# Performance work log

Measured on AMD Instinct MI355X. Metric: run time of the kernel, lower is better.

## Reference

```python
import jax, jax.numpy as jnp
import numpy as np
from jax import lax

PRE_NMS_THRESH = 0.05
PRE_NMS_TOP_N = 1000
FINAL_NMS_THRESH = 0.4  # hardcoded in forward(): boxlist_nms(..., 0.4)
MIN_SIZE = 0
STRIDE = 4.0
NEG = -1e9

N, C, H, W = 32, 1, 384, 384


def setup_inputs() -> dict:
    key = jax.random.key(0)
    k1, k2 = jax.random.split(key)
    box_cls = jax.random.uniform(k1, (N, C, H, W), dtype=jnp.float32)
    box_regression = jax.random.normal(k2, (N, 4, H, W), dtype=jnp.float32) * 20.0
    image_sizes = jnp.full((N, 2), H * int(STRIDE), dtype=jnp.int32)
    return {"box_cls": box_cls, "box_regression": box_regression, "image_sizes": image_sizes}


def decode_boxes(quad):
    # quad: [N, 4, H, W]; EAST geometry decode at stride 4 -> xyxy
    n, _, h, w = quad.shape
    x = (jnp.arange(w, dtype=quad.dtype) * STRIDE)[None, :]   # [1, W]
    y = (jnp.arange(h, dtype=quad.dtype) * STRIDE)[:, None]   # [H, 1]
    ymin = y - quad[:, 0]
    xmax = x + quad[:, 1]
    ymax = y + quad[:, 2]
    xmin = x - quad[:, 3]
    return jnp.stack([xmin, ymin, xmax, ymax], axis=1)  # [N, 4, H, W] (permute (3,0,1,2))


def iou_matrix(b):
    # b: [K, 4] xyxy
    x1, y1, x2, y2 = b[:, 0], b[:, 1], b[:, 2], b[:, 3]
    area = jnp.clip(x2 - x1, 0) * jnp.clip(y2 - y1, 0)
    ix1 = jnp.maximum(x1[:, None], x1[None, :])
    iy1 = jnp.maximum(y1[:, None], y1[None, :])
    ix2 = jnp.minimum(x2[:, None], x2[None, :])
    iy2 = jnp.minimum(y2[:, None], y2[None, :])
    inter = jnp.clip(ix2 - ix1, 0) * jnp.clip(iy2 - iy1, 0)
    union = area[:, None] + area[None, :] - inter
    return inter / jnp.maximum(union, 1e-9)


def greedy_nms(boxes, init_keep):
    # boxes: [K, 4] sorted by descending score; init_keep: [K] bool
    K = boxes.shape[0]
    iou = iou_matrix(boxes)
    idx = jnp.arange(K)

    def body(i, keep):
        suppress = (iou[i] > FINAL_NMS_THRESH) & (idx > i)
        return jnp.where(keep[i], keep & ~suppress, keep)

    return lax.fori_loop(0, K, body, init_keep)


def _forward(box_cls, box_regression):
    n, c, h, w = box_cls.shape
    boxes = decode_boxes(box_regression)                       # [N, 4, H, W]
    boxes = boxes.transpose(0, 2, 3, 1).reshape(n, h * w, 4)   # [N, HW, 4]
    scores = box_cls.transpose(0, 2, 3, 1).reshape(n, h * w)   # [N, HW] (C=1)

    # threshold + conditional top-k (padding with NEG emulates variable counts)
    masked = jnp.where(scores > PRE_NMS_THRESH, scores, NEG)
    scores_k, idx_k = lax.top_k(masked, PRE_NMS_TOP_N)         # [N, K], sorted desc
    boxes_k = jnp.take_along_axis(boxes, idx_k[..., None], axis=1)  # [N, K, 4]

    valid = scores_k > PRE_NMS_THRESH
    ws = boxes_k[..., 2] - boxes_k[..., 0]
    hs = boxes_k[..., 3] - boxes_k[..., 1]
    valid = valid & (ws >= MIN_SIZE) & (hs >= MIN_SIZE)        # remove_small_boxes

    keep = jax.vmap(greedy_nms)(boxes_k, valid)                # [N, K]
    out = jnp.concatenate([boxes_k, scores_k[..., None]], axis=-1)
    out = out * keep[..., None].astype(out.dtype)              # [N, K, 5]
    return out, keep


def reference(box_cls, box_regression, image_sizes):
    return _forward(box_cls, box_regression)
```

## Files before the change

kernel.cpp:

```cpp
#include <hip/hip_runtime.h>
#include <stdint.h>

#define NIMG 32
#define WID 384
#define HW 147456
#define TOPK 1000
#define KPAD 1024
#define NBINS 512
#define BIN_SCALEF 512.0f
#define SEGCAP 256
#define CANDCAP 2048
#define THRESH 0.05f
#define PREF_C 0.99f
#define NMS_T 0.4f
#define NBLK 18

typedef unsigned long long u64;
typedef unsigned int u32;

#define PCNT_OFF 0
#define PCAND_OFF 4096
#define SKEYS_OFF (PCAND_OFF + NIMG*NBLK*SEGCAP*8)
#define BOXES_OFF (SKEYS_OFF + NIMG*KPAD*8)

__device__ __forceinline__ float area_of(float x0, float y0, float x1, float y1) {
  float a = fmaxf(x1 - x0, 0.0f) * fmaxf(y1 - y0, 0.0f);
  asm volatile("" : "+v"(a));
  return a;
}

__device__ __forceinline__ bool iou_gt(float ax0, float ay0, float ax1, float ay1, float aa,
                                       float bx0, float by0, float bx1, float by1, float ba) {
  float ix1 = fmaxf(ax0, bx0);
  float iy1 = fmaxf(ay0, by0);
  float ix2 = fminf(ax1, bx1);
  float iy2 = fminf(ay1, by1);
  float iw = fmaxf(ix2 - ix1, 0.0f);
  float ih = fmaxf(iy2 - iy1, 0.0f);
  float inter = iw * ih;
  asm volatile("" : "+v"(inter));
  float uni = fmaxf(aa + ba - inter, 1e-9f);
  return (inter / uni) > NMS_T;
}

__device__ __forceinline__ u64 shflxor64(u64 v, int m) {
  int lo = __shfl_xor((int)(u32)v, m, 64);
  int hi = __shfl_xor((int)(u32)(v >> 32), m, 64);
  return ((u64)(u32)hi << 32) | (u32)lo;
}

__device__ __forceinline__ u64 make_key(float s, u32 idx) {
  u32 ord = __float_as_uint(s) | 0x80000000u;
  return ((u64)ord << 32) | (u32)(~idx);
}

__device__ __forceinline__ int bin_of(float s) {
  int b = (int)(s * BIN_SCALEF);
  return b < 0 ? 0 : (b > NBINS - 1 ? NBINS - 1 : b);
}

__global__ __launch_bounds__(256) void scan_kernel(const float* __restrict__ cls,
                                                   u32* __restrict__ pcnt,
                                                   u64* __restrict__ pcand) {
  __shared__ u64 lbuf[SEGCAP];
  __shared__ u32 lcnt;
  const int n = blockIdx.y;
  const int tid = threadIdx.x;
  const int lane = tid & 63;
  if (tid == 0) lcnt = 0;
  __syncthreads();

  const float4* src = (const float4*)(cls + (size_t)n * HW) + blockIdx.x * 2048;
  float4 A[8];
#pragma unroll
  for (int v = 0; v < 8; v++) A[v] = src[tid + v * 256];

  const u64 ltmask = (1ull << lane) - 1ull;
#pragma unroll
  for (int v = 0; v < 8; v++) {
    float ss[4] = {A[v].x, A[v].y, A[v].z, A[v].w};
#pragma unroll
    for (int c = 0; c < 4; c++) {
      float s = ss[c];
      bool pc = s > PREF_C;
      u64 m = __ballot(pc);
      if (m) {
        int ldr = __ffsll(m) - 1;
        u32 wb = 0;
        if (lane == ldr) wb = atomicAdd(&lcnt, (u32)__popcll(m));
        wb = (u32)__shfl((int)wb, ldr, 64);
        if (pc) {
          u32 pos = wb + (u32)__popcll(m & ltmask);
          if (pos < SEGCAP) lbuf[pos] = make_key(s, (u32)((blockIdx.x * 2048 + tid + v * 256) * 4 + c));
        }
      }
    }
  }
  __syncthreads();
  const int seg = n * NBLK + blockIdx.x;
  if (tid == 0) pcnt[seg] = (lcnt > SEGCAP) ? 0xFFFFFFFFu : lcnt;
  u32 c = lcnt < SEGCAP ? lcnt : (u32)SEGCAP;
  u64* pc = pcand + (size_t)seg * SEGCAP;
  for (u32 i = tid; i < c; i += 256) pc[i] = lbuf[i];
}

#define REGCHAIN(K, JSTART) do {                                            \
    const bool desc_ = ((tid & ((K) >> 1)) == 0);                           \
    for (int j_ = (JSTART); j_ >= 2; j_ >>= 1) {                            \
      int h_ = j_ >> 1;                                                     \
      bool low_ = (tid & h_) == 0;                                          \
      u64 p0_ = shflxor64(e0, h_), p1_ = shflxor64(e1, h_);                 \
      bool tm_ = (low_ == desc_);                                           \
      e0 = tm_ ? (e0 > p0_ ? e0 : p0_) : (e0 < p0_ ? e0 : p0_);             \
      e1 = tm_ ? (e1 > p1_ ? e1 : p1_) : (e1 < p1_ ? e1 : p1_);             \
    }                                                                       \
    { u64 lo_ = e0 < e1 ? e0 : e1, hi_ = e0 < e1 ? e1 : e0;                 \
      e0 = desc_ ? hi_ : lo_; e1 = desc_ ? lo_ : hi_; }                     \
  } while (0)

__global__ __launch_bounds__(1024) void sort_kernel(const float* __restrict__ cls,
                                                    const u32* __restrict__ pcnt,
                                                    const u64* __restrict__ pcand,
                                                    u64* __restrict__ skeys) {
  __shared__ u64 skey[CANDCAP];
  __shared__ u32 scnt[NBLK];
  __shared__ u32 soff[NBLK];
  __shared__ u32 bs[NBINS];
  __shared__ u32 stmp[64];
  __shared__ int stbin;
  __shared__ u32 sflag, sfc;

  const int n = blockIdx.x;
  const int tid = threadIdx.x;
  const int lane = tid & 63;
  const u64 ltmask = (1ull << lane) - 1ull;

  if (tid < NBLK) scnt[tid] = pcnt[n * NBLK + tid];
  skey[tid] = 0ull; skey[tid + 1024] = 0ull;
  if (tid == 0) sfc = 0;
  __syncthreads();
  if (tid == 0) {
    u32 f = 0, off = 0;
    for (int s = 0; s < NBLK; s++) {
      u32 c = scnt[s];
      if (c == 0xFFFFFFFFu) { f = 1; c = 0; }
      soff[s] = off; off += c;
    }
    if (off < TOPK || off > CANDCAP) f = 1;
    sflag = f;
  }
  __syncthreads();

  if (sflag == 0) {
    for (int s = 0; s < NBLK; s++) {
      u32 c = scnt[s];
      if (tid < c) skey[soff[s] + tid] = pcand[(size_t)(n * NBLK + s) * SEGCAP + tid];
    }
  } else {
    for (int i = tid; i < NBINS; i += 1024) bs[i] = 0;
    __syncthreads();
    const float* ci = cls + (size_t)n * HW;
    for (int base = 0; base < HW; base += 1024) {
      float s = ci[base + tid];
      if (s > THRESH) atomicAdd(&bs[bin_of(s)], 1u);
    }
    __syncthreads();
    if (tid < 64) {
      u32 cs = 0;
#pragma unroll
      for (int k2 = 0; k2 < 8; k2++) cs += bs[lane * 8 + k2];
      u32 s = cs;
#pragma unroll
      for (int d = 1; d < 64; d <<= 1) {
        u32 v = (u32)__shfl_down((int)s, d, 64);
        if (lane + d < 64) s += v;
      }
      stmp[lane] = s;
      u64 mask = __ballot(s >= TOPK);
      if (lane == 0) {
        int t = 0;
        if (mask) {
          int L = 63 - __clzll(mask);
          u32 acc = (L < 63) ? stmp[L + 1] : 0;
          for (int b = L * 8 + 7; b >= L * 8; b--) {
            acc += bs[b];
            if (acc >= TOPK) { t = b; break; }
          }
        }
        stbin = t;
      }
    }
    __syncthreads();
    const int t = stbin;
    for (int base = 0; base < HW; base += 1024) {
      int i = base + tid;
      float s = ci[i];
      bool p = (s > THRESH) && (bin_of(s) >= t);
      u64 m = __ballot(p);
      if (m) {
        int ldr = __ffsll(m) - 1;
        u32 wb = 0;
        if (lane == ldr) wb = atomicAdd(&sfc, (u32)__popcll(m));
        wb = (u32)__shfl((int)wb, ldr, 64);
        if (p) { u32 pos = wb + (u32)__popcll(m & ltmask); if (pos < CANDCAP) skey[pos] = make_key(s, (u32)i); }
      }
    }
  }
  __syncthreads();

  {
    u64 e0 = skey[2 * tid], e1 = skey[2 * tid + 1];
    REGCHAIN(2, 1); REGCHAIN(4, 2); REGCHAIN(8, 4); REGCHAIN(16, 8);
    REGCHAIN(32, 16); REGCHAIN(64, 32); REGCHAIN(128, 64);
    for (int k = 256; k <= CANDCAP; k <<= 1) {
      skey[2 * tid] = e0; skey[2 * tid + 1] = e1;
      __syncthreads();
      for (int j = k >> 1; j >= 128; j >>= 1) {
        int i = ((tid & ~(j - 1)) << 1) | (tid & (j - 1));
        u64 a = skey[i], b = skey[i + j];
        bool desc = ((i & k) == 0);
        if (desc ? (a < b) : (a > b)) { skey[i] = b; skey[i + j] = a; }
        __syncthreads();
      }
      e0 = skey[2 * tid]; e1 = skey[2 * tid + 1];
      REGCHAIN(k, 64);
    }
    skey[2 * tid] = e0; skey[2 * tid + 1] = e1;
    __syncthreads();
  }

  if (tid < KPAD) skeys[(size_t)n * KPAD + tid] = skey[tid];
}

__global__ __launch_bounds__(128) void decode_kernel(const float* __restrict__ reg,
                                                     const u64* __restrict__ skeys,
                                                     float4* __restrict__ gboxes) {
  const int n = blockIdx.y;
  const int s8 = blockIdx.x;
  const int tid = threadIdx.x;
  const int k = s8 * 128 + tid;
  u64 key = skeys[(size_t)n * KPAD + k];
  float x0 = 0.f, y0 = 0.f, x1 = 0.f, y1 = 0.f;
  if (key != 0ull && k < TOPK) {
    u32 idx = ~(u32)(key & 0xFFFFFFFFull);
    int iy = (int)idx / WID;
    int ix = (int)idx - iy * WID;
    float xx = (float)ix * 4.0f;
    float yy = (float)iy * 4.0f;
    const float* rb = reg + (size_t)n * 4 * HW;
    float r0 = rb[idx];
    float r1 = rb[HW + idx];
    float r2 = rb[2 * HW + idx];
    float r3 = rb[3 * HW + idx];
    y0 = yy - r0; x1 = xx + r1; y1 = yy + r2; x0 = xx - r3;
  }
  gboxes[(size_t)n * KPAD + k] = make_float4(x0, y0, x1, y1);
}

__global__ __launch_bounds__(1024) void nmsv_kernel(const float4* __restrict__ gboxes,
                                                    const u64* __restrict__ skeys,
                                                    float* __restrict__ out) {
  __shared__ float4 vbox[KPAD];
  __shared__ float varea[KPAD];
  __shared__ u64 mlds[136 * 64];
  __shared__ u32 wcnt[16], woff[16];
  __shared__ int pc[136], pk[136];
  __shared__ int sV, snch, snp;
  __shared__ u64 keepsh[16], srem[16];

  const int n = blockIdx.x;
  const int tid = threadIdx.x;
  const int lane = tid & 63;
  const int w = tid >> 6;
  const u64 ltmask = (1ull << lane) - 1ull;

  u64 key = skeys[(size_t)n * KPAD + tid];
  float4 b = gboxes[(size_t)n * KPAD + tid];
  float s = __uint_as_float((u32)(key >> 32) & 0x7FFFFFFFu);
  bool vb = (tid < TOPK) && (s > THRESH) && (b.z - b.x >= 0.0f) && (b.w - b.y >= 0.0f);
  vbox[tid] = make_float4(0.f, 0.f, 0.f, 0.f);
  varea[tid] = 0.0f;
  u64 vm = __ballot(vb);
  if (lane == 0) wcnt[w] = (u32)__popcll(vm);
  if (tid < 16) { srem[tid] = 0ull; keepsh[tid] = 0ull; }
  __syncthreads();
  if (tid == 0) {
    u32 off = 0;
    for (int i = 0; i < 16; i++) { woff[i] = off; off += wcnt[i]; }
    int V = (int)off;
    int nch = (V + 63) >> 6;
    sV = V; snch = nch; snp = nch * (nch + 1) / 2;
  }
  __syncthreads();
  const int V = sV, nch = snch, npairs = snp;

  int pos = -1;
  if (vb) {
    pos = (int)(woff[w] + (u32)__popcll(vm & ltmask));
    vbox[pos] = b;
    varea[pos] = area_of(b.x, b.y, b.z, b.w);
  }
  if (tid < npairs) {
    int p = tid, c = 0, base = 0;
    while (p >= base + (nch - c)) { base += nch - c; c++; }
    pc[tid] = c; pk[tid] = c + (p - base);
  }
  __syncthreads();

  for (int r = w; r < npairs * 64; r += 16) {
    int p = r >> 6, i = r & 63;
    int c = pc[p], k = pk[p];
    float4 rbx = vbox[k * 64 + i];
    float rarea = varea[k * 64 + i];
    float4 cbx = vbox[c * 64 + lane];
    float carea = varea[c * 64 + lane];
    bool pred = iou_gt(rbx.x, rbx.y, rbx.z, rbx.w, rarea,
                       cbx.x, cbx.y, cbx.z, cbx.w, carea);
    u64 m = __ballot(pred);
    if (lane == 0) mlds[r] = m;
  }
  __syncthreads();

  if (tid < 64) {
    for (int c = 0; c < nch; c++) {
      int pbase = c * nch - (c * (c - 1)) / 2 - c;
      u64 diag = mlds[(pbase + c) * 64 + lane];
      u64 ainit = (V >= (c + 1) * 64) ? ~0ull
                : ((V > c * 64) ? ((1ull << (V - c * 64)) - 1ull) : 0ull);
      u64 alive;
      {
        u64 a = ainit & ~srem[c];
        u32 alo2 = __builtin_amdgcn_readfirstlane((u32)a);
        u32 ahi2 = __builtin_amdgcn_readfirstlane((u32)(a >> 32));
        alive = ((u64)ahi2 << 32) | alo2;
      }
      u32 rlo = (u32)diag, rhi = (u32)(diag >> 32);
      u64 cur = alive;
      while (cur) {
        int i = __ffsll(cur) - 1;
        u32 rl = __builtin_amdgcn_readlane(rlo, i);
        u32 rh = __builtin_amdgcn_readlane(rhi, i);
        u64 rowi = ((u64)rh << 32) | rl;
        u64 lowmask = (i == 63) ? ~0ull : ((1ull << (i + 1)) - 1ull);
        rowi &= ~lowmask;
        alive &= ~rowi;
        cur &= ~rowi;
        cur &= cur - 1;
      }
      if (lane == 0) keepsh[c] = alive;
      const u64 K = alive;
      for (int k = c + 1; k < nch; k++) {
        bool sup = (mlds[(pbase + k) * 64 + lane] & K) != 0ull;
        u64 mres = __ballot(sup);
        if (lane == 0) srem[k] |= mres;
      }
    }
  }
  __syncthreads();

  u64 kb = (vb && pos >= 0) ? ((keepsh[pos >> 6] >> (pos & 63)) & 1ull) : 0ull;
  if (tid < TOPK) {
    float f = (float)kb;
    size_t ob = (size_t)n * (TOPK * 5) + (size_t)tid * 5;
    out[ob + 0] = kb ? b.x : 0.0f;
    out[ob + 1] = kb ? b.y : 0.0f;
    out[ob + 2] = kb ? b.z : 0.0f;
    out[ob + 3] = kb ? b.w : 0.0f;
    out[ob + 4] = kb ? s : 0.0f;
    out[(size_t)NIMG * TOPK * 5 + (size_t)n * TOPK + tid] = f;
  }
}

extern "C" void kernel_launch(void* const* d_in, const int* in_sizes, int n_in,
                              void* d_out, int out_size, void* d_ws, size_t ws_size,
                              hipStream_t stream) {
  const float* cls = (const float*)d_in[0];
  const float* reg = (const float*)d_in[1];
  float* out = (float*)d_out;

  uint8_t* ws = (uint8_t*)d_ws;
  u32* pcnt = (u32*)(ws + PCNT_OFF);
  u64* pcand = (u64*)(ws + PCAND_OFF);
  u64* skeys = (u64*)(ws + SKEYS_OFF);
  float4* gboxes = (float4*)(ws + BOXES_OFF);

  scan_kernel<<<dim3(NBLK, NIMG), 256, 0, stream>>>(cls, pcnt, pcand);
  sort_kernel<<<NIMG, 1024, 0, stream>>>(cls, pcnt, pcand, skeys);
  decode_kernel<<<dim3(8, NIMG), 128, 0, stream>>>(reg, skeys, gboxes);
  nmsv_kernel<<<NIMG, 1024, 0, stream>>>(gboxes, skeys, out);
}
```

Baseline: 172.9 us.

## Fuse sort, box decode and NMS into one per-image kernel

Merges the sort, decode and NMS kernels into a single 1024-thread block per image. Sorted keys stay in shared memory, and each thread decodes its own box directly from the regression tensor, so the skeys/gboxes workspace round-trips and two kernel launches go away. In exchange the block needs the sort and NMS shared-memory buffers together, which raises LDS usage. The decode also now runs with only 32 blocks in flight instead of 256.

```diff
diff --git a/kernel.cpp b/kernel.cpp
--- a/kernel.cpp
+++ b/kernel.cpp
@@ -20,8 +20,6 @@
 
 #define PCNT_OFF 0
 #define PCAND_OFF 4096
-#define SKEYS_OFF (PCAND_OFF + NIMG*NBLK*SEGCAP*8)
-#define BOXES_OFF (SKEYS_OFF + NIMG*KPAD*8)
 
 __device__ __forceinline__ float area_of(float x0, float y0, float x1, float y1) {
   float a = fmaxf(x1 - x0, 0.0f) * fmaxf(y1 - y0, 0.0f);
@@ -118,10 +116,11 @@
       e0 = desc_ ? hi_ : lo_; e1 = desc_ ? lo_ : hi_; }                     \
   } while (0)
 
-__global__ __launch_bounds__(1024) void sort_kernel(const float* __restrict__ cls,
-                                                    const u32* __restrict__ pcnt,
-                                                    const u64* __restrict__ pcand,
-                                                    u64* __restrict__ skeys) {
+__global__ __launch_bounds__(1024) void fused_kernel(const float* __restrict__ cls,
+                                                     const float* __restrict__ reg,
+                                                     const u32* __restrict__ pcnt,
+                                                     const u64* __restrict__ pcand,
+                                                     float* __restrict__ out) {
   __shared__ u64 skey[CANDCAP];
   __shared__ u32 scnt[NBLK];
   __shared__ u32 soff[NBLK];
@@ -129,6 +128,13 @@
   __shared__ u32 stmp[64];
   __shared__ int stbin;
   __shared__ u32 sflag, sfc;
+  __shared__ float4 vbox[KPAD];
+  __shared__ float varea[KPAD];
+  __shared__ u64 mlds[136 * 64];
+  __shared__ u32 wcnt[16], woff[16];
+  __shared__ int pc[136], pk[136];
+  __shared__ int sV, snch, snp;
+  __shared__ u64 keepsh[16], srem[16];
 
   const int n = blockIdx.x;
   const int tid = threadIdx.x;
@@ -229,19 +235,9 @@
     __syncthreads();
   }
 
-  if (tid < KPAD) skeys[(size_t)n * KPAD + tid] = skey[tid];
-}
-
-__global__ __launch_bounds__(128) void decode_kernel(const float* __restrict__ reg,
-                                                     const u64* __restrict__ skeys,
-                                                     float4* __restrict__ gboxes) {
-  const int n = blockIdx.y;
-  const int s8 = blockIdx.x;
-  const int tid = threadIdx.x;
-  const int k = s8 * 128 + tid;
-  u64 key = skeys[(size_t)n * KPAD + k];
-  float x0 = 0.f, y0 = 0.f, x1 = 0.f, y1 = 0.f;
-  if (key != 0ull && k < TOPK) {
+  u64 key = skey[tid];
+  float4 b = make_float4(0.f, 0.f, 0.f, 0.f);
+  if (key != 0ull && tid < TOPK) {
     u32 idx = ~(u32)(key & 0xFFFFFFFFull);
     int iy = (int)idx / WID;
     int ix = (int)idx - iy * WID;
@@ -252,34 +248,14 @@
     float r1 = rb[HW + idx];
     float r2 = rb[2 * HW + idx];
     float r3 = rb[3 * HW + idx];
-    y0 = yy - r0; x1 = xx + r1; y1 = yy + r2; x0 = xx - r3;
-  }
-  gboxes[(size_t)n * KPAD + k] = make_float4(x0, y0, x1, y1);
-}
-
-__global__ __launch_bounds__(1024) void nmsv_kernel(const float4* __restrict__ gboxes,
-                                                    const u64* __restrict__ skeys,
-                                                    float* __restrict__ out) {
-  __shared__ float4 vbox[KPAD];
-  __shared__ float varea[KPAD];
-  __shared__ u64 mlds[136 * 64];
-  __shared__ u32 wcnt[16], woff[16];
-  __shared__ int pc[136], pk[136];
-  __shared__ int sV, snch, snp;
-  __shared__ u64 keepsh[16], srem[16];
-
-  const int n = blockIdx.x;
-  const int tid = threadIdx.x;
-  const int lane = tid & 63;
-  const int w = tid >> 6;
-  const u64 ltmask = (1ull << lane) - 1ull;
-
-  u64 key = skeys[(size_t)n * KPAD + tid];
-  float4 b = gboxes[(size_t)n * KPAD + tid];
+    b.y = yy - r0; b.z = xx + r1; b.w = yy + r2; b.x = xx - r3;
+  }
   float s = __uint_as_float((u32)(key >> 32) & 0x7FFFFFFFu);
+
   bool vb = (tid < TOPK) && (s > THRESH) && (b.z - b.x >= 0.0f) && (b.w - b.y >= 0.0f);
   vbox[tid] = make_float4(0.f, 0.f, 0.f, 0.f);
   varea[tid] = 0.0f;
+  const int w = tid >> 6;
   u64 vm = __ballot(vb);
   if (lane == 0) wcnt[w] = (u32)__popcll(vm);
   if (tid < 16) { srem[tid] = 0ull; keepsh[tid] = 0ull; }
@@ -381,11 +357,7 @@
   uint8_t* ws = (uint8_t*)d_ws;
   u32* pcnt = (u32*)(ws + PCNT_OFF);
   u64* pcand = (u64*)(ws + PCAND_OFF);
-  u64* skeys = (u64*)(ws + SKEYS_OFF);
-  float4* gboxes = (float4*)(ws + BOXES_OFF);
 
   scan_kernel<<<dim3(NBLK, NIMG), 256, 0, stream>>>(cls, pcnt, pcand);
-  sort_kernel<<<NIMG, 1024, 0, stream>>>(cls, pcnt, pcand, skeys);
-  decode_kernel<<<dim3(8, NIMG), 128, 0, stream>>>(reg, skeys, gboxes);
-  nmsv_kernel<<<NIMG, 1024, 0, stream>>>(gboxes, skeys, out);
-}
+  fused_kernel<<<NIMG, 1024, 0, stream>>>(cls, reg, pcnt, pcand, out);
+}
```

Measured after the change: 177.8 us. 1.03x slower.
